# Kernel tuning notes

Measured on AMD Instinct MI355X. Metric: run time of the kernel, lower is better.

Reference implementation:

```python
import jax, jax.numpy as jnp
import numpy as np

B, S, D, O, E = 16, 512, 512, 512, 8


def setup_inputs() -> dict:
    key = jax.random.key(0)
    k1, k2, k3, k4, k5, k6 = jax.random.split(key, 6)
    x = jax.random.normal(k1, (B, S, D), dtype=jnp.float32)
    adj = jax.random.uniform(k2, (B, E, S, S), dtype=jnp.float32)
    # Stacked per-edge-type parameters (Gates: Linear(D,1); GraphConv: Linear(D,O))
    scale = 0.02
    Wg = jax.random.normal(k3, (E, D), dtype=jnp.float32) * scale  # gate weight, squeezed out-dim 1
    bg = jax.random.normal(k4, (E,), dtype=jnp.float32) * scale
    Wc = jax.random.normal(k5, (E, D, O), dtype=jnp.float32) * scale
    bc = jax.random.normal(k6, (E, O), dtype=jnp.float32) * scale
    return {"input": x, "adj": adj, "Wg": Wg, "bg": bg, "Wc": Wc, "bc": bc}


def reference(input, adj, Wg, bg, Wc, bc):
    # gate_status[e] = sigmoid(input @ Wg[e] + bg[e])  -> (B, E, S)
    gates = jax.nn.sigmoid(jnp.einsum('bsd,ed->bes', input, Wg) + bg[None, :, None])
    # h[e] = input @ Wc[e] + bc[e]                     -> (B, E, S, O)
    h = jnp.einsum('bsd,edo->beso', input, Wc) + bc[None, :, None, :]
    # adj_hat[e] = adj[:, e] * gates[e] broadcast over rows (gate of source node t)
    A = adj * gates[:, :, None, :]                     # (B, E, S, S)
    # sum over edge types of bmm(adj_hat, h), then relu
    out = jax.nn.relu(jnp.einsum('best,beto->bso', A, h))
    return out
```

## Files before the change

kernel.cpp:

```cpp
#include <hip/hip_runtime.h>
#include <stdint.h>

#define B_ 16
#define S_ 512
#define D_ 512
#define O_ 512
#define E_ 8

typedef unsigned short ushort_t;
typedef __attribute__((ext_vector_type(8))) short short8;
typedef __attribute__((ext_vector_type(8))) unsigned short ushort8;
typedef __attribute__((ext_vector_type(4))) unsigned short ushort4_t;
typedef __attribute__((ext_vector_type(4))) float f32x4;

__device__ __forceinline__ ushort_t f2bf(float f) {
  union { float f; unsigned int u; } v; v.f = f;
  unsigned int u = v.u;
  return (ushort_t)((u + 0x7fffu + ((u >> 16) & 1u)) >> 16);
}

__device__ __forceinline__ void gld_lds16(const void* g, void* l) {
  __builtin_amdgcn_global_load_lds((__attribute__((address_space(1))) void*)(g),
                                   (__attribute__((address_space(3))) void*)(l),
                                   16, 0, 0);
}


__global__ __launch_bounds__(256) void k_prep(const float* __restrict__ x,
                                              const float* __restrict__ Wg,
                                              const float* __restrict__ bg,
                                              float* __restrict__ gates,
                                              ushort_t* __restrict__ xb) {
  const int wave = threadIdx.x >> 6, lane = threadIdx.x & 63;
  const int row = blockIdx.x * 4 + wave;
  const float4* xr = (const float4*)(x + (size_t)row * D_);
  float4 x0 = xr[lane], x1 = xr[lane + 64];

  ushort4_t u0, u1;
  u0[0] = f2bf(x0.x); u0[1] = f2bf(x0.y); u0[2] = f2bf(x0.z); u0[3] = f2bf(x0.w);
  u1[0] = f2bf(x1.x); u1[1] = f2bf(x1.y); u1[2] = f2bf(x1.z); u1[3] = f2bf(x1.w);
  *(ushort4_t*)(xb + (size_t)row * D_ + 4 * lane) = u0;
  *(ushort4_t*)(xb + (size_t)row * D_ + 256 + 4 * lane) = u1;

  float p[E_];
#pragma unroll
  for (int e = 0; e < E_; ++e) {
    const float4* wr_ = (const float4*)(Wg + e * D_);
    float4 w0 = wr_[lane], w1 = wr_[lane + 64];
    p[e] = x0.x * w0.x + x0.y * w0.y + x0.z * w0.z + x0.w * w0.w +
           x1.x * w1.x + x1.y * w1.y + x1.z * w1.z + x1.w * w1.w;
  }
#pragma unroll
  for (int e = 0; e < E_; ++e) {
    float v = p[e];
#pragma unroll
    for (int off = 32; off > 0; off >>= 1) v += __shfl_xor(v, off, 64);
    p[e] = v;
  }
  const int b = row >> 9, s = row & (S_ - 1);
#pragma unroll
  for (int e = 0; e < E_; ++e)
    if (lane == e) {
      float z = p[e] + bg[e];
      gates[((size_t)(b * E_ + e)) * S_ + s] = 1.f / (1.f + __expf(-z));
    }
}

__global__ __launch_bounds__(256) void k_wcT(const float* __restrict__ Wc,
                                             ushort_t* __restrict__ WcT) {
  __shared__ float tile[64][65];
  const int e = blockIdx.z, d0 = blockIdx.y * 64, o0 = blockIdx.x * 64;
  const float* src = Wc + (size_t)e * D_ * O_;
#pragma unroll
  for (int i = 0; i < 16; ++i) {
    int idx = i * 256 + threadIdx.x;
    int r = idx >> 6, c = idx & 63;
    tile[r][c] = src[(size_t)(d0 + r) * O_ + o0 + c];
  }
  __syncthreads();
  ushort_t* dst = WcT + (size_t)e * O_ * D_;
#pragma unroll
  for (int i = 0; i < 16; ++i) {
    int idx = i * 256 + threadIdx.x;
    int r = idx >> 6, c = idx & 63;
    dst[(size_t)(o0 + r) * D_ + d0 + c] = f2bf(tile[c][r]);
  }
}


__global__ __launch_bounds__(256) void k_gemm1g(const ushort_t* __restrict__ WcT,
                                                const ushort_t* __restrict__ xb,
                                                const float* __restrict__ bc,
                                                const float* __restrict__ gates,
                                                ushort_t* __restrict__ hTg) {
  __shared__ __attribute__((aligned(16))) ushort_t lA[128 * 64];
  __shared__ __attribute__((aligned(16))) ushort_t lB[128 * 64];
  const int tid = threadIdx.x;
  const int m0 = blockIdx.x * 128, n0 = blockIdx.y * 128;
  const int tr = tid >> 3, tc = (tid & 7) * 8;
  const int lane = tid & 63, wid = tid >> 6;
  const int wr = wid >> 1, wc = wid & 1;
  const int lr = lane & 15, lk = (lane >> 4) * 8, lq = lane >> 4;

  f32x4 acc[4][4];
#pragma unroll
  for (int i = 0; i < 4; ++i)
#pragma unroll
    for (int j = 0; j < 4; ++j) acc[i][j] = (f32x4){0.f, 0.f, 0.f, 0.f};

  const ushort_t* gA = WcT + (size_t)(m0 + tr) * D_ + tc;
  const ushort_t* gB = xb + (size_t)(n0 + tr) * D_ + tc;

  for (int kk = 0; kk < 8; ++kk) {
    const int k0 = kk * 64;
    __syncthreads();
#pragma unroll
    for (int i = 0; i < 4; ++i) {
      gld_lds16(gA + (size_t)(32 * i) * D_ + k0, lA + tid * 8 + i * 2048);
      gld_lds16(gB + (size_t)(32 * i) * D_ + k0, lB + tid * 8 + i * 2048);
    }
    asm volatile("s_waitcnt vmcnt(0)" ::: "memory");
    __syncthreads();
    const ushort_t* pA = lA + (wr * 64 + lr) * 64 + lk;
    const ushort_t* pB = lB + (wc * 64 + lr) * 64 + lk;
#pragma unroll
    for (int ks = 0; ks < 2; ++ks) {
      short8 av[4], bv[4];
#pragma unroll
      for (int mi = 0; mi < 4; ++mi) av[mi] = *(const short8*)(pA + mi * 16 * 64 + ks * 32);
#pragma unroll
      for (int ni = 0; ni < 4; ++ni) bv[ni] = *(const short8*)(pB + ni * 16 * 64 + ks * 32);
#pragma unroll
      for (int mi = 0; mi < 4; ++mi)
#pragma unroll
        for (int ni = 0; ni < 4; ++ni)
          acc[mi][ni] = __builtin_amdgcn_mfma_f32_16x16x32_bf16(av[mi], bv[ni], acc[mi][ni], 0, 0, 0);
    }
  }

#pragma unroll
  for (int mi = 0; mi < 4; ++mi) {
    const int m_g = m0 + wr * 64 + mi * 16 + lq * 4;
    const int e = m_g >> 9;
#pragma unroll
    for (int ni = 0; ni < 4; ++ni) {
      const int n_g = n0 + wc * 64 + ni * 16 + lr;
      const int b = n_g >> 9, s = n_g & (S_ - 1);
      const float g = gates[((size_t)(b * E_ + e)) * S_ + s];
      f32x4 v = acc[mi][ni];
#pragma unroll
      for (int r = 0; r < 4; ++r)
        hTg[(size_t)(m_g + r) * (B_ * S_) + n_g] = f2bf((v[r] + bc[m_g + r]) * g);
    }
  }
}

template <int SPLIT>
__global__ __launch_bounds__(256, 4) void k_gemm2f(const float* __restrict__ adj,
                                                   const ushort_t* __restrict__ hTg,
                                                   float* __restrict__ dst) {
  __shared__ __attribute__((aligned(16))) ushort_t lA[128 * 64];
  __shared__ __attribute__((aligned(16))) ushort_t lB[128 * 64];
  const int tid = threadIdx.x;
  const int w = blockIdx.x;
  const int xcd = w & 7;
  const int r_ = w >> 3;
  const int xo = r_ & 3;
  const int yo = (r_ >> 2) & 3;
  const int zhi = r_ >> 4;
  const int z = xcd + 8 * zhi;
  const int b = z / SPLIT, sp = z % SPLIT;
  const int o0 = xo * 128, s0 = yo * 128;
  constexpr int EPB = E_ / SPLIT;
  const int tr = tid >> 3, tc = (tid & 7) * 8;
  const int lane = tid & 63, wid = tid >> 6;
  const int wr = wid >> 1, wc = wid & 1;
  const int lr = lane & 15, lk = (lane >> 4) * 8, lq = lane >> 4;

  f32x4 acc[4][4];
#pragma unroll
  for (int i = 0; i < 4; ++i)
#pragma unroll
    for (int j = 0; j < 4; ++j) acc[i][j] = (f32x4){0.f, 0.f, 0.f, 0.f};

  for (int kk = 0; kk < EPB * 8; ++kk) {
    const int e = sp * EPB + (kk >> 3), t0 = (kk & 7) * 64;
    const float* gAf = adj + ((size_t)((b * E_ + e) * S_ + s0 + tr)) * S_ + t0 + tc;
    float4 a0[4], a1[4];
#pragma unroll
    for (int i = 0; i < 4; ++i) {
      a0[i] = *(const float4*)(gAf + (size_t)(32 * i) * S_);
      a1[i] = *(const float4*)(gAf + (size_t)(32 * i) * S_ + 4);
    }
    __syncthreads();
#pragma unroll
    for (int i = 0; i < 4; ++i) {
      ushort8 wv;
      wv[0] = f2bf(a0[i].x); wv[1] = f2bf(a0[i].y);
      wv[2] = f2bf(a0[i].z); wv[3] = f2bf(a0[i].w);
      wv[4] = f2bf(a1[i].x); wv[5] = f2bf(a1[i].y);
      wv[6] = f2bf(a1[i].z); wv[7] = f2bf(a1[i].w);
      *(ushort8*)(lA + tid * 8 + i * 2048) = wv;
    }
    const ushort_t* gB = hTg + ((size_t)(e * O_ + o0 + tr)) * (B_ * S_) + b * S_ + t0 + tc;
#pragma unroll
    for (int i = 0; i < 4; ++i)
      gld_lds16(gB + (size_t)(32 * i) * (B_ * S_), lB + tid * 8 + i * 2048);
    asm volatile("s_waitcnt vmcnt(0)" ::: "memory");
    __syncthreads();
    const ushort_t* pA = lA + (wr * 64 + lr) * 64 + lk;
    const ushort_t* pB = lB + (wc * 64 + lr) * 64 + lk;
#pragma unroll
    for (int ks = 0; ks < 2; ++ks) {
      short8 av[4], bv[4];
#pragma unroll
      for (int mi = 0; mi < 4; ++mi) av[mi] = *(const short8*)(pA + mi * 16 * 64 + ks * 32);
#pragma unroll
      for (int ni = 0; ni < 4; ++ni) bv[ni] = *(const short8*)(pB + ni * 16 * 64 + ks * 32);
#pragma unroll
      for (int mi = 0; mi < 4; ++mi)
#pragma unroll
        for (int ni = 0; ni < 4; ++ni)
          acc[mi][ni] = __builtin_amdgcn_mfma_f32_16x16x32_bf16(av[mi], bv[ni], acc[mi][ni], 0, 0, 0);
    }
  }

  float* base = dst + ((size_t)sp * B_ + b) * S_ * O_;
#pragma unroll
  for (int mi = 0; mi < 4; ++mi) {
    const int s_g = s0 + wr * 64 + mi * 16 + lq * 4;
#pragma unroll
    for (int ni = 0; ni < 4; ++ni) {
      const int o_g = o0 + wc * 64 + ni * 16 + lr;
      f32x4 v = acc[mi][ni];
#pragma unroll
      for (int r = 0; r < 4; ++r) {
        float val = v[r];
        if (SPLIT == 1) val = fmaxf(val, 0.f);
        base[(size_t)(s_g + r) * O_ + o_g] = val;
      }
    }
  }
}

template <int SPLIT>
__global__ __launch_bounds__(256) void k_reduce(const float* __restrict__ part,
                                                float* __restrict__ out) {
  constexpr size_t N = (size_t)B_ * S_ * O_;
  size_t i4 = ((size_t)blockIdx.x * 256 + threadIdx.x) * 4;
  f32x4 a = *(const f32x4*)(part + i4);
#pragma unroll
  for (int s = 1; s < SPLIT; ++s) {
    f32x4 p = *(const f32x4*)(part + (size_t)s * N + i4);
    a[0] += p[0]; a[1] += p[1]; a[2] += p[2]; a[3] += p[3];
  }
  f32x4 o;
  o[0] = fmaxf(a[0], 0.f); o[1] = fmaxf(a[1], 0.f);
  o[2] = fmaxf(a[2], 0.f); o[3] = fmaxf(a[3], 0.f);
  *(f32x4*)(out + i4) = o;
}


extern "C" void kernel_launch(void* const* d_in, const int* in_sizes, int n_in,
                              void* d_out, int out_size, void* d_ws, size_t ws_size,
                              hipStream_t stream) {
  const float* x   = (const float*)d_in[0];
  const float* adj = (const float*)d_in[1];
  const float* Wg  = (const float*)d_in[2];
  const float* bg  = (const float*)d_in[3];
  const float* Wc  = (const float*)d_in[4];
  const float* bc  = (const float*)d_in[5];
  float* out = (float*)d_out;

  char* ws = (char*)d_ws;
  float* gates  = (float*)ws;    ws += (size_t)B_ * E_ * S_ * 4;
  ushort_t* xb  = (ushort_t*)ws; ws += (size_t)B_ * S_ * D_ * 2;
  ushort_t* WcT = (ushort_t*)ws; ws += (size_t)E_ * O_ * D_ * 2;
  ushort_t* hTg = (ushort_t*)ws; ws += (size_t)E_ * O_ * B_ * S_ * 2;
  float* part   = (float*)ws;
  const size_t base_bytes = (size_t)((char*)part - (char*)d_ws);
  const size_t part_sz = (size_t)B_ * S_ * O_ * sizeof(float);

  int split = 1;
  if (ws_size >= base_bytes + 4 * part_sz) split = 4;
  else if (ws_size >= base_bytes + 2 * part_sz) split = 2;

  k_prep<<<dim3((B_ * S_) / 4), dim3(256), 0, stream>>>(x, Wg, bg, gates, xb);
  k_wcT<<<dim3(O_ / 64, D_ / 64, E_), dim3(256), 0, stream>>>(Wc, WcT);
  k_gemm1g<<<dim3((E_ * O_) / 128, (B_ * S_) / 128), dim3(256), 0, stream>>>(WcT, xb, bc, gates, hTg);

  const int red_blocks = (int)(((size_t)B_ * S_ * O_) / (256 * 4));
  if (split == 4) {
    k_gemm2f<4><<<dim3(16 * B_ * 4), dim3(256), 0, stream>>>(adj, hTg, part);
    k_reduce<4><<<dim3(red_blocks), dim3(256), 0, stream>>>(part, out);
  } else if (split == 2) {
    k_gemm2f<2><<<dim3(16 * B_ * 2), dim3(256), 0, stream>>>(adj, hTg, part);
    k_reduce<2><<<dim3(red_blocks), dim3(256), 0, stream>>>(part, out);
  } else {
    k_gemm2f<1><<<dim3(16 * B_), dim3(256), 0, stream>>>(adj, hTg, out);
  }
}
```

Baseline: 181.9 us.

## Prefetch next adj tile into registers during MFMA compute in gemm2

Result: faster. 164.3 us (-9.7%).

```diff
diff --git a/kernel.cpp b/kernel.cpp
--- a/kernel.cpp
+++ b/kernel.cpp
@@ -23,6 +23,12 @@
   __builtin_amdgcn_global_load_lds((__attribute__((address_space(1))) void*)(g),
                                    (__attribute__((address_space(3))) void*)(l),
                                    16, 0, 0);
+}
+
+__device__ __forceinline__ f32x4 gload4(const float* p) {
+  f32x4 r;
+  asm volatile("global_load_dwordx4 %0, %1, off" : "=v"(r) : "v"(p));
+  return r;
 }
 
 
@@ -156,7 +162,7 @@
 }
 
 template <int SPLIT>
-__global__ __launch_bounds__(256, 4) void k_gemm2f(const float* __restrict__ adj,
+__global__ __launch_bounds__(256, 3) void k_gemm2f(const float* __restrict__ adj,
                                                    const ushort_t* __restrict__ hTg,
                                                    float* __restrict__ dst) {
   __shared__ __attribute__((aligned(16))) ushort_t lA[128 * 64];
@@ -172,6 +178,7 @@
   const int b = z / SPLIT, sp = z % SPLIT;
   const int o0 = xo * 128, s0 = yo * 128;
   constexpr int EPB = E_ / SPLIT;
+  constexpr int NKK = EPB * 8;
   const int tr = tid >> 3, tc = (tid & 7) * 8;
   const int lane = tid & 63, wid = tid >> 6;
   const int wr = wid >> 1, wc = wid & 1;
@@ -183,31 +190,52 @@
 #pragma unroll
     for (int j = 0; j < 4; ++j) acc[i][j] = (f32x4){0.f, 0.f, 0.f, 0.f};
 
-  for (int kk = 0; kk < EPB * 8; ++kk) {
+  f32x4 pf0, pf1, pf2, pf3, pf4, pf5, pf6, pf7;
+  {
+    const float* gAf = adj + ((size_t)((b * E_ + sp * EPB) * S_ + s0 + tr)) * S_ + tc;
+    pf0 = gload4(gAf + (size_t)(0 * 32) * S_);  pf1 = gload4(gAf + (size_t)(0 * 32) * S_ + 4);
+    pf2 = gload4(gAf + (size_t)(1 * 32) * S_);  pf3 = gload4(gAf + (size_t)(1 * 32) * S_ + 4);
+    pf4 = gload4(gAf + (size_t)(2 * 32) * S_);  pf5 = gload4(gAf + (size_t)(2 * 32) * S_ + 4);
+    pf6 = gload4(gAf + (size_t)(3 * 32) * S_);  pf7 = gload4(gAf + (size_t)(3 * 32) * S_ + 4);
+  }
+
+#pragma unroll 1
+  for (int kk = 0; kk < NKK; ++kk) {
+    asm volatile("s_waitcnt vmcnt(0)" ::: "memory");
+    __builtin_amdgcn_s_barrier();
+    __builtin_amdgcn_sched_barrier(0);
+
+#pragma unroll
+    for (int i = 0; i < 4; ++i) {
+      f32x4 lo = (i == 0) ? pf0 : (i == 1) ? pf2 : (i == 2) ? pf4 : pf6;
+      f32x4 hi = (i == 0) ? pf1 : (i == 1) ? pf3 : (i == 2) ? pf5 : pf7;
+      ushort8 wv;
+      wv[0] = f2bf(lo[0]); wv[1] = f2bf(lo[1]); wv[2] = f2bf(lo[2]); wv[3] = f2bf(lo[3]);
+      wv[4] = f2bf(hi[0]); wv[5] = f2bf(hi[1]); wv[6] = f2bf(hi[2]); wv[7] = f2bf(hi[3]);
+      *(ushort8*)(lA + tid * 8 + i * 2048) = wv;
+    }
+
     const int e = sp * EPB + (kk >> 3), t0 = (kk & 7) * 64;
-    const float* gAf = adj + ((size_t)((b * E_ + e) * S_ + s0 + tr)) * S_ + t0 + tc;
-    float4 a0[4], a1[4];
-#pragma unroll
-    for (int i = 0; i < 4; ++i) {
-      a0[i] = *(const float4*)(gAf + (size_t)(32 * i) * S_);
-      a1[i] = *(const float4*)(gAf + (size_t)(32 * i) * S_ + 4);
-    }
-    __syncthreads();
-#pragma unroll
-    for (int i = 0; i < 4; ++i) {
-      ushort8 wv;
-      wv[0] = f2bf(a0[i].x); wv[1] = f2bf(a0[i].y);
-      wv[2] = f2bf(a0[i].z); wv[3] = f2bf(a0[i].w);
-      wv[4] = f2bf(a1[i].x); wv[5] = f2bf(a1[i].y);
-      wv[6] = f2bf(a1[i].z); wv[7] = f2bf(a1[i].w);
-      *(ushort8*)(lA + tid * 8 + i * 2048) = wv;
-    }
     const ushort_t* gB = hTg + ((size_t)(e * O_ + o0 + tr)) * (B_ * S_) + b * S_ + t0 + tc;
 #pragma unroll
     for (int i = 0; i < 4; ++i)
       gld_lds16(gB + (size_t)(32 * i) * (B_ * S_), lB + tid * 8 + i * 2048);
-    asm volatile("s_waitcnt vmcnt(0)" ::: "memory");
-    __syncthreads();
+
+    if (kk + 1 < NKK) {
+      const int kn = kk + 1;
+      const int en = sp * EPB + (kn >> 3), tn = (kn & 7) * 64;
+      const float* gAf = adj + ((size_t)((b * E_ + en) * S_ + s0 + tr)) * S_ + tn + tc;
+      pf0 = gload4(gAf + (size_t)(0 * 32) * S_);  pf1 = gload4(gAf + (size_t)(0 * 32) * S_ + 4);
+      pf2 = gload4(gAf + (size_t)(1 * 32) * S_);  pf3 = gload4(gAf + (size_t)(1 * 32) * S_ + 4);
+      pf4 = gload4(gAf + (size_t)(2 * 32) * S_);  pf5 = gload4(gAf + (size_t)(2 * 32) * S_ + 4);
+      pf6 = gload4(gAf + (size_t)(3 * 32) * S_);  pf7 = gload4(gAf + (size_t)(3 * 32) * S_ + 4);
+      asm volatile("s_waitcnt vmcnt(8) lgkmcnt(0)" ::: "memory");
+    } else {
+      asm volatile("s_waitcnt vmcnt(0) lgkmcnt(0)" ::: "memory");
+    }
+    __builtin_amdgcn_s_barrier();
+    __builtin_amdgcn_sched_barrier(0);
+
     const ushort_t* pA = lA + (wr * 64 + lr) * 64 + lk;
     const ushort_t* pB = lB + (wc * 64 + lr) * 64 + lk;
 #pragma unroll
```

## Software-pipeline adj/hTg loads in gemm2 with double-buffered LDS and swizzle

Applied to the files above, without the earlier changes.

Measured after the change: 160.2 us. 11.9% less time.

```diff
diff --git a/kernel.cpp b/kernel.cpp
--- a/kernel.cpp
+++ b/kernel.cpp
@@ -12,11 +12,18 @@
 typedef __attribute__((ext_vector_type(8))) unsigned short ushort8;
 typedef __attribute__((ext_vector_type(4))) unsigned short ushort4_t;
 typedef __attribute__((ext_vector_type(4))) float f32x4;
+typedef __attribute__((ext_vector_type(4))) unsigned int u32x4;
 
 __device__ __forceinline__ ushort_t f2bf(float f) {
   union { float f; unsigned int u; } v; v.f = f;
   unsigned int u = v.u;
   return (ushort_t)((u + 0x7fffu + ((u >> 16) & 1u)) >> 16);
+}
+
+__device__ __forceinline__ unsigned int cvtpk(float lo, float hi) {
+  unsigned int r;
+  asm("v_cvt_pk_bf16_f32 %0, %1, %2" : "=v"(r) : "v"(lo), "v"(hi));
+  return r;
 }
 
 __device__ __forceinline__ void gld_lds16(const void* g, void* l) {
@@ -155,12 +162,84 @@
   }
 }
 
+
+#define LOAD_PFA(KIDX)                                                               \
+  {                                                                                  \
+    const int e_ = sp * EPB + ((KIDX) >> 3), t_ = ((KIDX) & 7) * 64;                 \
+    const float* g_ = adj + ((size_t)((b * E_ + e_) * S_ + s0 + tr)) * S_ + t_ + tcf;\
+    pf0 = *(const float4*)(g_);            pf1 = *(const float4*)(g_ + 4);           \
+    pf2 = *(const float4*)(g_ + 32 * S_);  pf3 = *(const float4*)(g_ + 32 * S_ + 4); \
+    pf4 = *(const float4*)(g_ + 64 * S_);  pf5 = *(const float4*)(g_ + 64 * S_ + 4); \
+    pf6 = *(const float4*)(g_ + 96 * S_);  pf7 = *(const float4*)(g_ + 96 * S_ + 4); \
+  }
+
+#define ISSUE_B(BUF, KIDX)                                                           \
+  {                                                                                  \
+    const int e_ = sp * EPB + ((KIDX) >> 3), t_ = ((KIDX) & 7) * 64;                 \
+    const ushort_t* g_ = hTg + ((size_t)(e_ * O_ + o0 + tr)) * (B_ * S_) +           \
+                         b * S_ + t_ + chS * 8;                                      \
+    gld_lds16(g_ + (size_t)0 * (B_ * S_),  &lB[BUF][tid * 8 + 0 * 2048]);            \
+    gld_lds16(g_ + (size_t)32 * (B_ * S_), &lB[BUF][tid * 8 + 1 * 2048]);            \
+    gld_lds16(g_ + (size_t)64 * (B_ * S_), &lB[BUF][tid * 8 + 2 * 2048]);            \
+    gld_lds16(g_ + (size_t)96 * (B_ * S_), &lB[BUF][tid * 8 + 3 * 2048]);            \
+  }
+
+#define SUBITER(KK, RBUF, DONEXT, VM)                                                \
+  {                                                                                  \
+    __builtin_amdgcn_s_barrier();                                                    \
+    __builtin_amdgcn_sched_barrier(0);                                               \
+    {                                    \
+      u32x4 w_;                                                                      \
+      w_[0] = cvtpk(pf0.x, pf0.y); w_[1] = cvtpk(pf0.z, pf0.w);                      \
+      w_[2] = cvtpk(pf1.x, pf1.y); w_[3] = cvtpk(pf1.z, pf1.w);                      \
+      *(u32x4*)(lA + 0 * 2048 + wrA) = w_;                                           \
+      w_[0] = cvtpk(pf2.x, pf2.y); w_[1] = cvtpk(pf2.z, pf2.w);                      \
+      w_[2] = cvtpk(pf3.x, pf3.y); w_[3] = cvtpk(pf3.z, pf3.w);                      \
+      *(u32x4*)(lA + 1 * 2048 + wrA) = w_;                                           \
+      w_[0] = cvtpk(pf4.x, pf4.y); w_[1] = cvtpk(pf4.z, pf4.w);                      \
+      w_[2] = cvtpk(pf5.x, pf5.y); w_[3] = cvtpk(pf5.z, pf5.w);                      \
+      *(u32x4*)(lA + 2 * 2048 + wrA) = w_;                                           \
+      w_[0] = cvtpk(pf6.x, pf6.y); w_[1] = cvtpk(pf6.z, pf6.w);                      \
+      w_[2] = cvtpk(pf7.x, pf7.y); w_[3] = cvtpk(pf7.z, pf7.w);                      \
+      *(u32x4*)(lA + 3 * 2048 + wrA) = w_;                                           \
+    }                                                                                \
+    if (DONEXT) {                                                                    \
+      LOAD_PFA((KK) + 1);                                                            \
+      ISSUE_B((RBUF) ^ 1, (KK) + 1);                                                 \
+    }                                                                                \
+    asm volatile("s_waitcnt vmcnt(" #VM ") lgkmcnt(0)" ::: "memory");                \
+    __builtin_amdgcn_sched_barrier(0);                                               \
+    __builtin_amdgcn_s_barrier();                                                    \
+    __builtin_amdgcn_sched_barrier(0);                                               \
+    {                                                                                \
+      const ushort_t* pA_ = lA + (wr * 64 + lr) * 64;                                \
+      const ushort_t* pB_ = &lB[RBUF][(wc * 64 + lr) * 64];                          \
+      __builtin_amdgcn_s_setprio(1);                                                 \
+      _Pragma("unroll")                                                              \
+      for (int ks = 0; ks < 2; ++ks) {                                               \
+        const int co_ = ks ? cks1 : cks0;                                            \
+        short8 av[4], bv[4];                                                         \
+        _Pragma("unroll")                                                            \
+        for (int mi = 0; mi < 4; ++mi) av[mi] = *(const short8*)(pA_ + mi * 1024 + co_);\
+        _Pragma("unroll")                                                            \
+        for (int ni = 0; ni < 4; ++ni) bv[ni] = *(const short8*)(pB_ + ni * 1024 + co_);\
+        _Pragma("unroll")                                                            \
+        for (int mi = 0; mi < 4; ++mi)                                               \
+          _Pragma("unroll")                                                          \
+          for (int ni = 0; ni < 4; ++ni)                                             \
+            acc[mi][ni] = __builtin_amdgcn_mfma_f32_16x16x32_bf16(av[mi], bv[ni],    \
+                                                                  acc[mi][ni], 0, 0, 0);\
+      }                                                                              \
+      __builtin_amdgcn_s_setprio(0);                                                 \
+    }                                                                                \
+  }
+
 template <int SPLIT>
-__global__ __launch_bounds__(256, 4) void k_gemm2f(const float* __restrict__ adj,
+__global__ __launch_bounds__(256, 3) void k_gemm2f(const float* __restrict__ adj,
                                                    const ushort_t* __restrict__ hTg,
                                                    float* __restrict__ dst) {
   __shared__ __attribute__((aligned(16))) ushort_t lA[128 * 64];
-  __shared__ __attribute__((aligned(16))) ushort_t lB[128 * 64];
+  __shared__ __attribute__((aligned(16))) ushort_t lB[2][128 * 64];
   const int tid = threadIdx.x;
   const int w = blockIdx.x;
   const int xcd = w & 7;
@@ -172,10 +251,17 @@
   const int b = z / SPLIT, sp = z % SPLIT;
   const int o0 = xo * 128, s0 = yo * 128;
   constexpr int EPB = E_ / SPLIT;
-  const int tr = tid >> 3, tc = (tid & 7) * 8;
+  constexpr int NKK = EPB * 8;
+  const int tr = tid >> 3;
+  const int tcf = (tid & 7) * 8;
+  const int chS = (tid & 7) ^ (tr & 7);
+  const int wrA = tr * 64 + chS * 8;
   const int lane = tid & 63, wid = tid >> 6;
   const int wr = wid >> 1, wc = wid & 1;
-  const int lr = lane & 15, lk = (lane >> 4) * 8, lq = lane >> 4;
+  const int lr = lane & 15, lq = lane >> 4;
+  const int rsw = lane & 7;
+  const int cks0 = (((lane >> 4) + 0) ^ rsw) * 8;
+  const int cks1 = (((lane >> 4) + 4) ^ rsw) * 8;
 
   f32x4 acc[4][4];
 #pragma unroll
@@ -183,47 +269,18 @@
 #pragma unroll
     for (int j = 0; j < 4; ++j) acc[i][j] = (f32x4){0.f, 0.f, 0.f, 0.f};
 
-  for (int kk = 0; kk < EPB * 8; ++kk) {
-    const int e = sp * EPB + (kk >> 3), t0 = (kk & 7) * 64;
-    const float* gAf = adj + ((size_t)((b * E_ + e) * S_ + s0 + tr)) * S_ + t0 + tc;
-    float4 a0[4], a1[4];
-#pragma unroll
-    for (int i = 0; i < 4; ++i) {
-      a0[i] = *(const float4*)(gAf + (size_t)(32 * i) * S_);
-      a1[i] = *(const float4*)(gAf + (size_t)(32 * i) * S_ + 4);
-    }
-    __syncthreads();
-#pragma unroll
-    for (int i = 0; i < 4; ++i) {
-      ushort8 wv;
-      wv[0] = f2bf(a0[i].x); wv[1] = f2bf(a0[i].y);
-      wv[2] = f2bf(a0[i].z); wv[3] = f2bf(a0[i].w);
-      wv[4] = f2bf(a1[i].x); wv[5] = f2bf(a1[i].y);
-      wv[6] = f2bf(a1[i].z); wv[7] = f2bf(a1[i].w);
-      *(ushort8*)(lA + tid * 8 + i * 2048) = wv;
-    }
-    const ushort_t* gB = hTg + ((size_t)(e * O_ + o0 + tr)) * (B_ * S_) + b * S_ + t0 + tc;
-#pragma unroll
-    for (int i = 0; i < 4; ++i)
-      gld_lds16(gB + (size_t)(32 * i) * (B_ * S_), lB + tid * 8 + i * 2048);
-    asm volatile("s_waitcnt vmcnt(0)" ::: "memory");
-    __syncthreads();
-    const ushort_t* pA = lA + (wr * 64 + lr) * 64 + lk;
-    const ushort_t* pB = lB + (wc * 64 + lr) * 64 + lk;
-#pragma unroll
-    for (int ks = 0; ks < 2; ++ks) {
-      short8 av[4], bv[4];
-#pragma unroll
-      for (int mi = 0; mi < 4; ++mi) av[mi] = *(const short8*)(pA + mi * 16 * 64 + ks * 32);
-#pragma unroll
-      for (int ni = 0; ni < 4; ++ni) bv[ni] = *(const short8*)(pB + ni * 16 * 64 + ks * 32);
-#pragma unroll
-      for (int mi = 0; mi < 4; ++mi)
-#pragma unroll
-        for (int ni = 0; ni < 4; ++ni)
-          acc[mi][ni] = __builtin_amdgcn_mfma_f32_16x16x32_bf16(av[mi], bv[ni], acc[mi][ni], 0, 0, 0);
-    }
-  }
+  float4 pf0, pf1, pf2, pf3, pf4, pf5, pf6, pf7;
+
+  LOAD_PFA(0);
+  ISSUE_B(0, 0);
+
+#pragma unroll 1
+  for (int kk = 0; kk < NKK - 2; kk += 2) {
+    SUBITER(kk, 0, 1, 12)
+    SUBITER(kk + 1, 1, 1, 12)
+  }
+  SUBITER(NKK - 2, 0, 1, 12)
+  SUBITER(NKK - 1, 1, 0, 0)
 
   float* base = dst + ((size_t)sp * B_ + b) * S_ * O_;
 #pragma unroll
```
